# Kernel optimization log

Hardware: AMD Instinct MI355X
Metric: run time of the kernel (lower is better)

Reference implementation:

```python
import jax, jax.numpy as jnp
import numpy as np

D_MODEL, D_STATE, EXPAND = 1024, 256, 2
BATCH, SEQ = 8, 2048


def setup_inputs() -> dict:
    key = jax.random.key(0)
    ks = jax.random.split(key, 7)
    s = 0.02
    return {
        "x": jax.random.normal(ks[0], (BATCH, SEQ, D_MODEL), jnp.float32),
        "W_in": jax.random.normal(ks[1], (D_MODEL, D_MODEL * EXPAND), jnp.float32) * s,
        "b_in": jax.random.normal(ks[2], (D_MODEL * EXPAND,), jnp.float32) * s,
        "W_state": jax.random.normal(ks[3], (D_MODEL * EXPAND, D_STATE), jnp.float32) * s,
        "b_state": jax.random.normal(ks[4], (D_STATE,), jnp.float32) * s,
        "W_out": jax.random.normal(ks[5], (D_STATE, D_MODEL), jnp.float32) * s,
        "b_out": jax.random.normal(ks[6], (D_MODEL,), jnp.float32) * s,
        "init_state": jnp.zeros((1, D_STATE), jnp.float32),
    }


def reference(x, W_in, b_in, W_state, b_state, W_out, b_out, init_state):
    # x: [B, T, D]
    x_proj = jax.nn.silu(jnp.einsum("btd,de->bte", x, W_in) + b_in)  # [B,T,2D]
    # state_proj depends only on x_proj, so batch the GEMM over all timesteps
    updates = jnp.einsum("bte,es->bts", x_proj, W_state) + b_state    # [B,T,S]
    updates_t = jnp.swapaxes(updates, 0, 1)                            # [T,B,S]
    state0 = jnp.broadcast_to(init_state, (x.shape[0], init_state.shape[1]))

    def step(state, u):
        new = jax.nn.silu(state + u)
        return new, new

    _, states = jax.lax.scan(step, state0, updates_t)  # [T,B,S]
    out = jnp.einsum("tbs,sd->tbd", states, W_out) + b_out  # [T,B,D]
    return jnp.swapaxes(out, 0, 1)  # [B,T,D]
```

## Files before the change

kernel.cpp:

```cpp
#include <hip/hip_runtime.h>
#include <cstdint>
#include <cstddef>

#define BATCH 8
#define SEQ   2048
#define DM    1024
#define DE    2048
#define DSZ   256
#define MROWS (BATCH*SEQ)
#define MCHUNK 8192

typedef _Float16 f16;
typedef _Float16 f16x4 __attribute__((ext_vector_type(4)));
typedef _Float16 f16x8 __attribute__((ext_vector_type(8)));
typedef float  f32x4  __attribute__((ext_vector_type(4)));

__device__ __forceinline__ void glds16(const void* gp, void* lp) {
  __builtin_amdgcn_global_load_lds(
      (const __attribute__((address_space(1))) void*)gp,
      (__attribute__((address_space(3))) void*)lp, 16, 0, 0);
}

__device__ __forceinline__ float silu_f(float x) {
  return x * __builtin_amdgcn_rcpf(1.0f + __expf(-x));
}

__device__ __forceinline__ int swz(int k8, int r) { return k8 ^ ((r >> 1) & 3); }

__global__ void split_x_k(const float* __restrict__ in, f16* __restrict__ oh,
                          f16* __restrict__ ol, int n) {
  int i = (blockIdx.x * blockDim.x + threadIdx.x) * 4;
  const int stride = gridDim.x * blockDim.x * 4;
  for (; i < n; i += stride) {
    float4 v = *(const float4*)(in + i);
    f16x4 h, l;
    h[0] = (f16)v.x; l[0] = (f16)(v.x - (float)h[0]);
    h[1] = (f16)v.y; l[1] = (f16)(v.y - (float)h[1]);
    h[2] = (f16)v.z; l[2] = (f16)(v.z - (float)h[2]);
    h[3] = (f16)v.w; l[3] = (f16)(v.w - (float)h[3]);
    *(f16x4*)(oh + i) = h;
    *(f16x4*)(ol + i) = l;
  }
}

__global__ void transpose_split_k(const float* __restrict__ in, f16* __restrict__ oh,
                                  f16* __restrict__ ol, int R, int C) {
  __shared__ float tile[32][33];
  const int c0 = blockIdx.x * 32, r0 = blockIdx.y * 32;
  const int tx = threadIdx.x, ty = threadIdx.y;
  #pragma unroll
  for (int i = 0; i < 4; ++i)
    tile[ty + i*8][tx] = in[(size_t)(r0 + ty + i*8) * C + c0 + tx];
  __syncthreads();
  #pragma unroll
  for (int i = 0; i < 4; ++i) {
    float v = tile[tx][ty + i*8];
    f16 h = (f16)v;
    size_t idx = (size_t)(c0 + ty + i*8) * R + r0 + tx;
    oh[idx] = h;
    ol[idx] = (f16)(v - (float)h);
  }
}

__global__ void transpose_cast_f16_k(const float* __restrict__ in, f16* __restrict__ out, int R, int C) {
  __shared__ float tile[32][33];
  const int c0 = blockIdx.x * 32, r0 = blockIdx.y * 32;
  const int tx = threadIdx.x, ty = threadIdx.y;
  #pragma unroll
  for (int i = 0; i < 4; ++i)
    tile[ty + i*8][tx] = in[(size_t)(r0 + ty + i*8) * C + c0 + tx];
  __syncthreads();
  #pragma unroll
  for (int i = 0; i < 4; ++i)
    out[(size_t)(c0 + ty + i*8) * R + r0 + tx] = (f16)tile[tx][ty + i*8];
}

__global__ __launch_bounds__(512) void gemm1_k(const f16* __restrict__ Ah, const f16* __restrict__ Al,
                                               const f16* __restrict__ Bh, const f16* __restrict__ Bl,
                                               const float* __restrict__ bias,
                                               f16* __restrict__ Ch, f16* __restrict__ Cl) {
  const int K = 1024, N = 2048;
  __shared__ f16 sAh[2][4096], sAl[2][4096], sBh[2][4096], sBl[2][4096];

  const int tid = threadIdx.x;
  const int w = tid >> 6, l = tid & 63;
  const int bid = blockIdx.x;
  const int xcd = bid & 7, loc = bid >> 3;
  const int mt = xcd * 8 + (loc & 7);
  const int nt = loc >> 3;
  const int bm = mt * 128, bn = nt * 128;
  const int wm = (w >> 2) * 64, wn = (w & 3) * 32;
  const int lr = l & 15, lq = l >> 4;

  const int r = tid >> 2, k8 = swz(tid & 3, r);
  const f16* pAh = Ah + (size_t)(bm + r) * K + k8 * 8;
  const f16* pAl = Al + (size_t)(bm + r) * K + k8 * 8;
  const f16* pBh = Bh + (size_t)(bn + r) * K + k8 * 8;
  const f16* pBl = Bl + (size_t)(bn + r) * K + k8 * 8;
  const int dst = tid * 8;

  int offA[4], offB[2];
  #pragma unroll
  for (int i = 0; i < 4; ++i) {
    const int row = wm + i*16 + lr;
    offA[i] = row * 32 + swz(lq, row) * 8;
  }
  #pragma unroll
  for (int j = 0; j < 2; ++j) {
    const int row = wn + j*16 + lr;
    offB[j] = row * 32 + swz(lq, row) * 8;
  }

  f32x4 acc[4][2] = {};

  glds16(pAh, &sAh[0][dst]); glds16(pAl, &sAl[0][dst]);
  glds16(pBh, &sBh[0][dst]); glds16(pBl, &sBl[0][dst]);
  pAh += 32; pAl += 32; pBh += 32; pBl += 32;
  __syncthreads();

  for (int kt = 0; kt < 32; ++kt) {
    const int cur = kt & 1;
    if (kt < 31) {
      const int nxt = cur ^ 1;
      glds16(pAh, &sAh[nxt][dst]); glds16(pAl, &sAl[nxt][dst]);
      glds16(pBh, &sBh[nxt][dst]); glds16(pBl, &sBl[nxt][dst]);
      pAh += 32; pAl += 32; pBh += 32; pBl += 32;
    }
    f16x8 ah[4], al[4], bh[2], bl[2];
    #pragma unroll
    for (int i = 0; i < 4; ++i) {
      ah[i] = *(const f16x8*)(&sAh[cur][0] + offA[i]);
      al[i] = *(const f16x8*)(&sAl[cur][0] + offA[i]);
    }
    #pragma unroll
    for (int j = 0; j < 2; ++j) {
      bh[j] = *(const f16x8*)(&sBh[cur][0] + offB[j]);
      bl[j] = *(const f16x8*)(&sBl[cur][0] + offB[j]);
    }
    __builtin_amdgcn_s_setprio(1);
    #pragma unroll
    for (int i = 0; i < 4; ++i)
      #pragma unroll
      for (int j = 0; j < 2; ++j) {
        acc[i][j] = __builtin_amdgcn_mfma_f32_16x16x32_f16(ah[i], bh[j], acc[i][j], 0, 0, 0);
        acc[i][j] = __builtin_amdgcn_mfma_f32_16x16x32_f16(ah[i], bl[j], acc[i][j], 0, 0, 0);
        acc[i][j] = __builtin_amdgcn_mfma_f32_16x16x32_f16(al[i], bh[j], acc[i][j], 0, 0, 0);
      }
    __builtin_amdgcn_s_setprio(0);
    __syncthreads();
  }

  #pragma unroll
  for (int j = 0; j < 2; ++j) {
    const int col = bn + wn + j*16 + lr;
    const float bv = bias[col];
    #pragma unroll
    for (int i = 0; i < 4; ++i)
      #pragma unroll
      for (int r4 = 0; r4 < 4; ++r4) {
        const int row = bm + wm + i*16 + lq*4 + r4;
        const float s = silu_f(acc[i][j][r4] + bv);
        const f16 h = (f16)s;
        const size_t idx = (size_t)row * N + col;
        Ch[idx] = h;
        Cl[idx] = (f16)(s - (float)h);
      }
  }
}

__global__ __launch_bounds__(256) void gemm2s_k(const f16* __restrict__ Ah, const f16* __restrict__ Al,
                                                const f16* __restrict__ Bh, const f16* __restrict__ Bl,
                                                const float* __restrict__ bias,
                                                float* __restrict__ C) {
  const int K = 2048, N = 256;
  __shared__ f16 sAh[2][2][2048], sAl[2][2][2048], sBh[2][2][2048], sBl[2][2][2048];

  const int tid = threadIdx.x;
  const int w = tid >> 6, l = tid & 63;
  const int bid = blockIdx.x;
  const int bm = (bid & 127) * 64;
  const int bn = (bid >> 7) * 64;
  const int wm = (w & 1) * 32, wn = (w >> 1) * 32;
  const int lr = l & 15, lq = l >> 4;

  const int r = tid >> 2, k8 = swz(tid & 3, r);
  const f16* pAh = Ah + (size_t)(bm + r) * K + k8 * 8;
  const f16* pAl = Al + (size_t)(bm + r) * K + k8 * 8;
  const f16* pBh = Bh + (size_t)(bn + r) * K + k8 * 8;
  const f16* pBl = Bl + (size_t)(bn + r) * K + k8 * 8;
  const int dst = tid * 8;

  int offA[2], offB[2];
  #pragma unroll
  for (int i = 0; i < 2; ++i) {
    const int row = wm + i*16 + lr;
    offA[i] = row * 32 + swz(lq, row) * 8;
  }
  #pragma unroll
  for (int j = 0; j < 2; ++j) {
    const int row = wn + j*16 + lr;
    offB[j] = row * 32 + swz(lq, row) * 8;
  }

  f32x4 acc[2][2] = {};

  glds16(pAh,      &sAh[0][0][dst]); glds16(pAh + 32, &sAh[0][1][dst]);
  glds16(pAl,      &sAl[0][0][dst]); glds16(pAl + 32, &sAl[0][1][dst]);
  glds16(pBh,      &sBh[0][0][dst]); glds16(pBh + 32, &sBh[0][1][dst]);
  glds16(pBl,      &sBl[0][0][dst]); glds16(pBl + 32, &sBl[0][1][dst]);
  pAh += 64; pAl += 64; pBh += 64; pBl += 64;
  __syncthreads();

  for (int kt = 0; kt < 32; ++kt) {
    const int cur = kt & 1;
    if (kt < 31) {
      const int nxt = cur ^ 1;
      glds16(pAh,      &sAh[nxt][0][dst]); glds16(pAh + 32, &sAh[nxt][1][dst]);
      glds16(pAl,      &sAl[nxt][0][dst]); glds16(pAl + 32, &sAl[nxt][1][dst]);
      glds16(pBh,      &sBh[nxt][0][dst]); glds16(pBh + 32, &sBh[nxt][1][dst]);
      glds16(pBl,      &sBl[nxt][0][dst]); glds16(pBl + 32, &sBl[nxt][1][dst]);
      pAh += 64; pAl += 64; pBh += 64; pBl += 64;
    }
    #pragma unroll
    for (int s = 0; s < 2; ++s) {
      f16x8 ah[2], al[2], bh[2], bl[2];
      #pragma unroll
      for (int i = 0; i < 2; ++i) {
        ah[i] = *(const f16x8*)(&sAh[cur][s][0] + offA[i]);
        al[i] = *(const f16x8*)(&sAl[cur][s][0] + offA[i]);
      }
      #pragma unroll
      for (int j = 0; j < 2; ++j) {
        bh[j] = *(const f16x8*)(&sBh[cur][s][0] + offB[j]);
        bl[j] = *(const f16x8*)(&sBl[cur][s][0] + offB[j]);
      }
      __builtin_amdgcn_s_setprio(1);
      #pragma unroll
      for (int i = 0; i < 2; ++i)
        #pragma unroll
        for (int j = 0; j < 2; ++j) {
          acc[i][j] = __builtin_amdgcn_mfma_f32_16x16x32_f16(ah[i], bh[j], acc[i][j], 0, 0, 0);
          acc[i][j] = __builtin_amdgcn_mfma_f32_16x16x32_f16(ah[i], bl[j], acc[i][j], 0, 0, 0);
          acc[i][j] = __builtin_amdgcn_mfma_f32_16x16x32_f16(al[i], bh[j], acc[i][j], 0, 0, 0);
        }
      __builtin_amdgcn_s_setprio(0);
    }
    __syncthreads();
  }

  #pragma unroll
  for (int j = 0; j < 2; ++j) {
    const int col = bn + wn + j*16 + lr;
    const float bv = bias[col];
    #pragma unroll
    for (int i = 0; i < 2; ++i)
      #pragma unroll
      for (int r4 = 0; r4 < 4; ++r4) {
        const int row = bm + wm + i*16 + lq*4 + r4;
        C[(size_t)row * N + col] = acc[i][j][r4] + bv;
      }
  }
}

__global__ __launch_bounds__(256) void gemm3_k(const f16* __restrict__ A,
                                               const f16* __restrict__ Bt,
                                               const float* __restrict__ bias,
                                               float* __restrict__ C) {
  const int K = 256, N = 1024;
  __shared__ f16 sA[2][4096], sB[2][4096];

  const int tid = threadIdx.x;
  const int w = tid >> 6, l = tid & 63;
  const int bm = blockIdx.y * 128, bn = blockIdx.x * 128;
  const int wm = (w >> 1) * 64, wn = (w & 1) * 64;
  const int lr = l & 15, lq = l >> 4;

  const f16 *pA[2], *pB[2]; int dstc[2];
  #pragma unroll
  for (int p = 0; p < 2; ++p) {
    const int c = p * 256 + tid;
    const int r = c >> 2, k8 = swz(c & 3, r);
    pA[p] = A  + (size_t)(bm + r) * K + k8 * 8;
    pB[p] = Bt + (size_t)(bn + r) * K + k8 * 8;
    dstc[p] = c * 8;
  }

  int offA[4], offB[4];
  #pragma unroll
  for (int i = 0; i < 4; ++i) {
    const int rowA = wm + i*16 + lr;
    const int rowB = wn + i*16 + lr;
    offA[i] = rowA * 32 + swz(lq, rowA) * 8;
    offB[i] = rowB * 32 + swz(lq, rowB) * 8;
  }

  f32x4 acc[4][4] = {};

  glds16(pA[0], &sA[0][dstc[0]]); glds16(pA[1], &sA[0][dstc[1]]);
  glds16(pB[0], &sB[0][dstc[0]]); glds16(pB[1], &sB[0][dstc[1]]);
  pA[0] += 32; pA[1] += 32; pB[0] += 32; pB[1] += 32;
  __syncthreads();

  for (int kt = 0; kt < 8; ++kt) {
    const int cur = kt & 1;
    if (kt < 7) {
      const int nxt = cur ^ 1;
      glds16(pA[0], &sA[nxt][dstc[0]]); glds16(pA[1], &sA[nxt][dstc[1]]);
      glds16(pB[0], &sB[nxt][dstc[0]]); glds16(pB[1], &sB[nxt][dstc[1]]);
      pA[0] += 32; pA[1] += 32; pB[0] += 32; pB[1] += 32;
    }
    f16x8 af[4], bfr[4];
    #pragma unroll
    for (int i = 0; i < 4; ++i) af[i]  = *(const f16x8*)(&sA[cur][0] + offA[i]);
    #pragma unroll
    for (int j = 0; j < 4; ++j) bfr[j] = *(const f16x8*)(&sB[cur][0] + offB[j]);
    __builtin_amdgcn_s_setprio(1);
    #pragma unroll
    for (int i = 0; i < 4; ++i)
      #pragma unroll
      for (int j = 0; j < 4; ++j)
        acc[i][j] = __builtin_amdgcn_mfma_f32_16x16x32_f16(af[i], bfr[j], acc[i][j], 0, 0, 0);
    __builtin_amdgcn_s_setprio(0);
    __syncthreads();
  }

  #pragma unroll
  for (int j = 0; j < 4; ++j) {
    const int col = bn + wn + j*16 + lr;
    const float bv = bias[col];
    #pragma unroll
    for (int i = 0; i < 4; ++i)
      #pragma unroll
      for (int r4 = 0; r4 < 4; ++r4) {
        const int row = bm + wm + i*16 + lq*4 + r4;
        C[(size_t)row * N + col] = acc[i][j][r4] + bv;
      }
  }
}

#define L2E 1.4426950408889634f
__global__ __launch_bounds__(64) void scan_k(const float* __restrict__ upd,
                                             const float* __restrict__ init,
                                             f16* __restrict__ states) {
  const int b = blockIdx.x >> 2, sq = blockIdx.x & 3;
  const int s = sq * 64 + threadIdx.x;
  const float* u = upd + (size_t)b * SEQ * DSZ + s;
  f16* st = states + (size_t)b * SEQ * DSZ + s;
  float state = init[s];

  float r0[16], r1[16], r2[16], ulog[16];
  #pragma unroll
  for (int i = 0; i < 16; ++i) r0[i] = u[(size_t)i * DSZ];
  #pragma unroll
  for (int i = 0; i < 16; ++i) r1[i] = u[(size_t)(16 + i) * DSZ];
  #pragma unroll
  for (int i = 0; i < 16; ++i) ulog[i] = r0[i] * (-L2E);

  for (int t0 = 0; t0 < SEQ; t0 += 16) {
    if (t0 + 32 < SEQ) {
      #pragma unroll
      for (int i = 0; i < 16; ++i) r2[i] = u[(size_t)(t0 + 32 + i) * DSZ];
    }
    f16 res[16];
    #pragma unroll
    for (int i = 0; i < 16; ++i) {
      const float e = __builtin_amdgcn_exp2f(__builtin_fmaf(state, -L2E, ulog[i]));
      const float x = state + r0[i];
      state = x * __builtin_amdgcn_rcpf(1.0f + e);
      res[i] = (f16)state;
    }
    #pragma unroll
    for (int i = 0; i < 16; ++i) st[(size_t)(t0 + i) * DSZ] = res[i];
    #pragma unroll
    for (int i = 0; i < 16; ++i) { r0[i] = r1[i]; ulog[i] = r1[i] * (-L2E); r1[i] = r2[i]; }
  }
}

extern "C" void kernel_launch(void* const* d_in, const int* in_sizes, int n_in,
                              void* d_out, int out_size, void* d_ws, size_t ws_size,
                              hipStream_t stream) {
  const float* x       = (const float*)d_in[0];
  const float* W_in    = (const float*)d_in[1];
  const float* b_in    = (const float*)d_in[2];
  const float* W_state = (const float*)d_in[3];
  const float* b_state = (const float*)d_in[4];
  const float* W_out   = (const float*)d_in[5];
  const float* b_out   = (const float*)d_in[6];
  const float* init_st = (const float*)d_in[7];
  float* out = (float*)d_out;

  char* ws = (char*)d_ws;
  f16*   xh        = (f16*)(ws + 0);
  f16*   xl        = (f16*)(ws + 33554432);
  f16*   xproj_h   = (f16*)(ws + 67108864);
  f16*   xproj_l   = (f16*)(ws + 100663296);
  float* upd       = (float*)(ws + 134217728);
  f16*   states    = (f16*)(ws + 150994944);
  f16*   w_in_h    = (f16*)(ws + 159383552);
  f16*   w_in_l    = (f16*)(ws + 163577856);
  f16*   w_state_h = (f16*)(ws + 167772160);
  f16*   w_state_l = (f16*)(ws + 168820736);
  f16*   w_out_t   = (f16*)(ws + 169869312);

  split_x_k<<<4096, 256, 0, stream>>>(x, xh, xl, MROWS * DM);
  dim3 tb(32, 8);
  transpose_split_k<<<dim3(DE/32,  DM/32), tb, 0, stream>>>(W_in,    w_in_h,    w_in_l,    DM,  DE);
  transpose_split_k<<<dim3(DSZ/32, DE/32), tb, 0, stream>>>(W_state, w_state_h, w_state_l, DE,  DSZ);
  transpose_cast_f16_k<<<dim3(DM/32, DSZ/32), tb, 0, stream>>>(W_out, w_out_t, DSZ, DM);

  for (int c = 0; c < 2; ++c) {
    const size_t ro = (size_t)c * MCHUNK;
    gemm1_k<<<1024, 512, 0, stream>>>(
        xh + ro * DM, xl + ro * DM, w_in_h, w_in_l, b_in, xproj_h, xproj_l);
    gemm2s_k<<<512, 256, 0, stream>>>(
        xproj_h, xproj_l, w_state_h, w_state_l, b_state, upd + ro * DSZ);
  }

  scan_k<<<BATCH*4, 64, 0, stream>>>(upd, init_st, states);

  gemm3_k<<<dim3(DM/128, MROWS/128), 256, 0, stream>>>(states, w_out_t, b_out, out);
}
```

Baseline: 555.3 us.

## Enlarge gemm1 tiles to 256x256 with split-precision K-segment pipelining

gemm1 now uses 256x256 block tiles (8 waves, each 128x64) instead of 128x128. The three hi/lo f16 products are folded into a single K loop of 48 steps, where segments choose Ah/Al and Bh/Bl sources. Staging is interleaved in quarter-steps with explicit vmcnt waits and raw barriers. The aim is more operand reuse per LDS byte and overlap of global-to-LDS loads with MFMA. In exchange it costs many more accumulator registers, a larger LDS footprint, and only 256 blocks per chunk, so the grid may underfill the CUs.

Result: slower. 608.3 us (+9.5%).

```diff
diff --git a/kernel.cpp b/kernel.cpp
--- a/kernel.cpp
+++ b/kernel.cpp
@@ -75,87 +75,147 @@
     out[(size_t)(c0 + ty + i*8) * R + r0 + tx] = (f16)tile[tx][ty + i*8];
 }
 
-__global__ __launch_bounds__(512) void gemm1_k(const f16* __restrict__ Ah, const f16* __restrict__ Al,
-                                               const f16* __restrict__ Bh, const f16* __restrict__ Bl,
-                                               const float* __restrict__ bias,
-                                               f16* __restrict__ Ch, f16* __restrict__ Cl) {
+__global__ __launch_bounds__(512, 2) void gemm1_k(const f16* __restrict__ Ah, const f16* __restrict__ Al,
+                                                  const f16* __restrict__ Bh, const f16* __restrict__ Bl,
+                                                  const float* __restrict__ bias,
+                                                  f16* __restrict__ Ch, f16* __restrict__ Cl) {
   const int K = 1024, N = 2048;
-  __shared__ f16 sAh[2][4096], sAl[2][4096], sBh[2][4096], sBl[2][4096];
+  __shared__ f16 sA[2][2][8192];
+  __shared__ f16 sB[2][2][8192];
 
   const int tid = threadIdx.x;
   const int w = tid >> 6, l = tid & 63;
   const int bid = blockIdx.x;
   const int xcd = bid & 7, loc = bid >> 3;
-  const int mt = xcd * 8 + (loc & 7);
-  const int nt = loc >> 3;
-  const int bm = mt * 128, bn = nt * 128;
-  const int wm = (w >> 2) * 64, wn = (w & 3) * 32;
+  const int mt = xcd * 4 + (loc & 3);
+  const int nt = loc >> 2;
+  const int bm = mt * 256, bn = nt * 256;
+  const int wm = (w >> 2) * 128, wn = (w & 3) * 64;
   const int lr = l & 15, lq = l >> 4;
 
-  const int r = tid >> 2, k8 = swz(tid & 3, r);
-  const f16* pAh = Ah + (size_t)(bm + r) * K + k8 * 8;
-  const f16* pAl = Al + (size_t)(bm + r) * K + k8 * 8;
-  const f16* pBh = Bh + (size_t)(bn + r) * K + k8 * 8;
-  const f16* pBl = Bl + (size_t)(bn + r) * K + k8 * 8;
-  const int dst = tid * 8;
-
-  int offA[4], offB[2];
-  #pragma unroll
-  for (int i = 0; i < 4; ++i) {
+  const int rA0 = tid >> 2,        k8A0 = swz(tid & 3, rA0);
+  const int rA1 = 128 + (tid >> 2), k8A1 = swz(tid & 3, rA1);
+  const size_t baseA0 = (size_t)(bm + rA0) * K + k8A0 * 8;
+  const size_t baseA1 = (size_t)(bm + rA1) * K + k8A1 * 8;
+  const size_t baseB0 = (size_t)(bn + rA0) * K + k8A0 * 8;
+  const size_t baseB1 = (size_t)(bn + rA1) * K + k8A1 * 8;
+  const int dst0 = tid * 8, dst1 = (512 + tid) * 8;
+
+  auto stageA = [&](int t, int s) {
+    const int seg = t >> 4;
+    const int koff = (t & 15) * 64 + s * 32;
+    const f16* src = (seg < 2 ? Ah : Al);
+    f16* d = &sA[t & 1][s][0];
+    glds16(src + baseA0 + koff, d + dst0);
+    glds16(src + baseA1 + koff, d + dst1);
+  };
+  auto stageB = [&](int t, int s) {
+    const int seg = t >> 4;
+    const int koff = (t & 15) * 64 + s * 32;
+    const f16* src = (seg == 1 ? Bl : Bh);
+    f16* d = &sB[t & 1][s][0];
+    glds16(src + baseB0 + koff, d + dst0);
+    glds16(src + baseB1 + koff, d + dst1);
+  };
+
+  int offA[8], offB[4];
+  #pragma unroll
+  for (int i = 0; i < 8; ++i) {
     const int row = wm + i*16 + lr;
     offA[i] = row * 32 + swz(lq, row) * 8;
   }
   #pragma unroll
-  for (int j = 0; j < 2; ++j) {
+  for (int j = 0; j < 4; ++j) {
     const int row = wn + j*16 + lr;
     offB[j] = row * 32 + swz(lq, row) * 8;
   }
 
-  f32x4 acc[4][2] = {};
-
-  glds16(pAh, &sAh[0][dst]); glds16(pAl, &sAl[0][dst]);
-  glds16(pBh, &sBh[0][dst]); glds16(pBl, &sBl[0][dst]);
-  pAh += 32; pAl += 32; pBh += 32; pBl += 32;
+  f32x4 acc[8][4] = {};
+
+  stageA(0, 0); stageB(0, 0); stageA(0, 1); stageB(0, 1);
   __syncthreads();
 
-  for (int kt = 0; kt < 32; ++kt) {
-    const int cur = kt & 1;
-    if (kt < 31) {
-      const int nxt = cur ^ 1;
-      glds16(pAh, &sAh[nxt][dst]); glds16(pAl, &sAl[nxt][dst]);
-      glds16(pBh, &sBh[nxt][dst]); glds16(pBl, &sBl[nxt][dst]);
-      pAh += 32; pAl += 32; pBh += 32; pBl += 32;
-    }
-    f16x8 ah[4], al[4], bh[2], bl[2];
-    #pragma unroll
-    for (int i = 0; i < 4; ++i) {
-      ah[i] = *(const f16x8*)(&sAh[cur][0] + offA[i]);
-      al[i] = *(const f16x8*)(&sAl[cur][0] + offA[i]);
-    }
-    #pragma unroll
-    for (int j = 0; j < 2; ++j) {
-      bh[j] = *(const f16x8*)(&sBh[cur][0] + offB[j]);
-      bl[j] = *(const f16x8*)(&sBl[cur][0] + offB[j]);
-    }
+  for (int kt = 0; kt < 48; ++kt) {
+    const int slot = kt & 1;
+    const f16* bA0 = &sA[slot][0][0];
+    const f16* bA1 = &sA[slot][1][0];
+    const f16* bB0 = &sB[slot][0][0];
+    const f16* bB1 = &sB[slot][1][0];
+    f16x8 a[4], bf[4];
+
+    if (kt < 47) { stageA(kt + 1, 0); asm volatile("s_waitcnt vmcnt(6)" ::: "memory"); }
+    else         {                    asm volatile("s_waitcnt vmcnt(4)" ::: "memory"); }
+    __builtin_amdgcn_s_barrier();
+    asm volatile("" ::: "memory");
+    #pragma unroll
+    for (int j = 0; j < 4; ++j) bf[j] = *(const f16x8*)(bB0 + offB[j]);
+    #pragma unroll
+    for (int i = 0; i < 4; ++i) a[i] = *(const f16x8*)(bA0 + offA[i]);
     __builtin_amdgcn_s_setprio(1);
     #pragma unroll
     for (int i = 0; i < 4; ++i)
       #pragma unroll
-      for (int j = 0; j < 2; ++j) {
-        acc[i][j] = __builtin_amdgcn_mfma_f32_16x16x32_f16(ah[i], bh[j], acc[i][j], 0, 0, 0);
-        acc[i][j] = __builtin_amdgcn_mfma_f32_16x16x32_f16(ah[i], bl[j], acc[i][j], 0, 0, 0);
-        acc[i][j] = __builtin_amdgcn_mfma_f32_16x16x32_f16(al[i], bh[j], acc[i][j], 0, 0, 0);
-      }
+      for (int j = 0; j < 4; ++j)
+        acc[i][j] = __builtin_amdgcn_mfma_f32_16x16x32_f16(a[i], bf[j], acc[i][j], 0, 0, 0);
     __builtin_amdgcn_s_setprio(0);
-    __syncthreads();
-  }
-
-  #pragma unroll
-  for (int j = 0; j < 2; ++j) {
+    asm volatile("" ::: "memory");
+    __builtin_amdgcn_s_barrier();
+
+    if (kt < 47) stageB(kt + 1, 0);
+    __builtin_amdgcn_s_barrier();
+    asm volatile("" ::: "memory");
+    #pragma unroll
+    for (int i = 0; i < 4; ++i) a[i] = *(const f16x8*)(bA0 + offA[4 + i]);
+    __builtin_amdgcn_s_setprio(1);
+    #pragma unroll
+    for (int i = 0; i < 4; ++i)
+      #pragma unroll
+      for (int j = 0; j < 4; ++j)
+        acc[4 + i][j] = __builtin_amdgcn_mfma_f32_16x16x32_f16(a[i], bf[j], acc[4 + i][j], 0, 0, 0);
+    __builtin_amdgcn_s_setprio(0);
+    asm volatile("" ::: "memory");
+    __builtin_amdgcn_s_barrier();
+
+    if (kt < 47) { stageA(kt + 1, 1); asm volatile("s_waitcnt vmcnt(6)" ::: "memory"); }
+    else         {                    asm volatile("s_waitcnt vmcnt(0)" ::: "memory"); }
+    __builtin_amdgcn_s_barrier();
+    asm volatile("" ::: "memory");
+    #pragma unroll
+    for (int j = 0; j < 4; ++j) bf[j] = *(const f16x8*)(bB1 + offB[j]);
+    #pragma unroll
+    for (int i = 0; i < 4; ++i) a[i] = *(const f16x8*)(bA1 + offA[i]);
+    __builtin_amdgcn_s_setprio(1);
+    #pragma unroll
+    for (int i = 0; i < 4; ++i)
+      #pragma unroll
+      for (int j = 0; j < 4; ++j)
+        acc[i][j] = __builtin_amdgcn_mfma_f32_16x16x32_f16(a[i], bf[j], acc[i][j], 0, 0, 0);
+    __builtin_amdgcn_s_setprio(0);
+    asm volatile("" ::: "memory");
+    __builtin_amdgcn_s_barrier();
+
+    if (kt < 47) stageB(kt + 1, 1);
+    __builtin_amdgcn_s_barrier();
+    asm volatile("" ::: "memory");
+    #pragma unroll
+    for (int i = 0; i < 4; ++i) a[i] = *(const f16x8*)(bA1 + offA[4 + i]);
+    __builtin_amdgcn_s_setprio(1);
+    #pragma unroll
+    for (int i = 0; i < 4; ++i)
+      #pragma unroll
+      for (int j = 0; j < 4; ++j)
+        acc[4 + i][j] = __builtin_amdgcn_mfma_f32_16x16x32_f16(a[i], bf[j], acc[4 + i][j], 0, 0, 0);
+    __builtin_amdgcn_s_setprio(0);
+    asm volatile("" ::: "memory");
+    __builtin_amdgcn_s_barrier();
+  }
+
+  #pragma unroll
+  for (int j = 0; j < 4; ++j) {
     const int col = bn + wn + j*16 + lr;
     const float bv = bias[col];
     #pragma unroll
-    for (int i = 0; i < 4; ++i)
+    for (int i = 0; i < 8; ++i)
       #pragma unroll
       for (int r4 = 0; r4 < 4; ++r4) {
         const int row = bm + wm + i*16 + lq*4 + r4;
@@ -410,7 +470,7 @@
 
   for (int c = 0; c < 2; ++c) {
     const size_t ro = (size_t)c * MCHUNK;
-    gemm1_k<<<1024, 512, 0, stream>>>(
+    gemm1_k<<<256, 512, 0, stream>>>(
         xh + ro * DM, xl + ro * DM, w_in_h, w_in_l, b_in, xproj_h, xproj_l);
     gemm2s_k<<<512, 256, 0, stream>>>(
         xproj_h, xproj_l, w_state_h, w_state_l, b_state, upd + ro * DSZ);
```
